# Optimization experiments

Measured on AMD Instinct MI355X. Metric: run time of the kernel, lower is better.

The kernel has to match this reference:

```python
import jax, jax.numpy as jnp
import numpy as np

B, S, E, H = 4, 2048, 1024, 16
D = E // H
LR_MULT = 100.0
EPS = 1e-5

def setup_inputs() -> dict:
    key = jax.random.key(0)
    ks = jax.random.split(key, 4)
    x = jax.random.normal(ks[0], (B, S, E), dtype=jnp.float32)
    # nn.MultiheadAttention in_proj_weight [3E,E], out_proj.weight [E,E] (bias=False)
    W_qkv = jax.random.normal(ks[1], (3 * E, E), dtype=jnp.float32) * (1.0 / np.sqrt(E))
    W_o = jax.random.normal(ks[2], (E, E), dtype=jnp.float32) * (1.0 / np.sqrt(E))
    ln_w = jnp.ones((E,), dtype=jnp.float32)
    scaler = jnp.asarray(1.0 / LR_MULT, dtype=jnp.float32)
    return {"x": x, "W_qkv": W_qkv, "W_o": W_o, "ln_w": ln_w, "scaler": scaler}

def _layernorm(x, w):
    mu = jnp.mean(x, axis=-1, keepdims=True)
    var = jnp.mean(jnp.square(x - mu), axis=-1, keepdims=True)
    return (x - mu) * jax.lax.rsqrt(var + EPS) * w

def reference(x, W_qkv, W_o, ln_w, scaler):
    resid = x
    xn = _layernorm(x, ln_w)
    qkv = jnp.einsum('bse,fe->bsf', xn, W_qkv)  # [B,S,3E]
    q, k, v = jnp.split(qkv, 3, axis=-1)
    q = q.reshape(B, S, H, D)
    k = k.reshape(B, S, H, D)
    v = v.reshape(B, S, H, D)
    scores = jnp.einsum('bihd,bjhd->bhij', q, k) / jnp.sqrt(jnp.asarray(D, x.dtype))
    # linear_encoding_base[i,j] = j - i; bias = softplus(100*scaler)*(j-i) where j<=i else -inf
    i_idx = jnp.arange(S)
    rel = (i_idx[None, :] - i_idx[:, None]).astype(x.dtype)  # j - i
    causal = i_idx[None, :] <= i_idx[:, None]                # tril: j <= i
    slope = jax.nn.softplus(LR_MULT * scaler)
    bias = jnp.where(causal, slope * rel, -jnp.inf)          # [S,S]
    att = jax.nn.softmax(scores + bias[None, None, :, :], axis=-1)
    out = jnp.einsum('bhij,bjhd->bihd', att, v).reshape(B, S, E)
    out = jnp.einsum('bse,fe->bsf', out, W_o)
    return out + resid
```

## Files before the change

kernel.cpp:

```cpp
#include <hip/hip_runtime.h>

typedef unsigned short u16;
typedef unsigned int u32;
typedef __bf16 bf16x8 __attribute__((ext_vector_type(8)));
typedef float f32x4 __attribute__((ext_vector_type(4)));

#define B_ 4
#define S_ 2048
#define E_ 1024
#define H_ 16
#define D_ 64

__device__ __forceinline__ u16 f2bf(float f) {
  u32 u = __float_as_uint(f);
  u32 r = u + 0x7fffu + ((u >> 16) & 1u);
  return (u16)(r >> 16);
}

__device__ __forceinline__ void gload16(const u16* g, u16* l) {
  __builtin_amdgcn_global_load_lds((const __attribute__((address_space(1))) void*)g,
                                   (__attribute__((address_space(3))) void*)l, 16, 0, 0);
}

__global__ __launch_bounds__(256) void ln_kernel(const float* __restrict__ x,
                                                 const float* __restrict__ w,
                                                 u16* __restrict__ xn) {
  const int lane = threadIdx.x & 63;
  const int wv = threadIdx.x >> 6;
  const int row = blockIdx.x * 4 + wv;
  const float4* xr = (const float4*)(x + (size_t)row * E_);
  float4 vv[4];
  float s = 0.f, sq = 0.f;
#pragma unroll
  for (int i = 0; i < 4; ++i) {
    vv[i] = xr[lane + i * 64];
    s += vv[i].x + vv[i].y + vv[i].z + vv[i].w;
    sq += vv[i].x * vv[i].x + vv[i].y * vv[i].y + vv[i].z * vv[i].z + vv[i].w * vv[i].w;
  }
#pragma unroll
  for (int off = 1; off < 64; off <<= 1) {
    s += __shfl_xor(s, off);
    sq += __shfl_xor(sq, off);
  }
  const float mu = s * (1.f / E_);
  const float rs = rsqrtf(sq * (1.f / E_) - mu * mu + 1e-5f);
  u16* xo = xn + (size_t)row * E_;
  const float4* wr = (const float4*)w;
#pragma unroll
  for (int i = 0; i < 4; ++i) {
    float4 w4 = wr[lane + i * 64];
    ushort4 o;
    o.x = f2bf((vv[i].x - mu) * rs * w4.x);
    o.y = f2bf((vv[i].y - mu) * rs * w4.y);
    o.z = f2bf((vv[i].z - mu) * rs * w4.z);
    o.w = f2bf((vv[i].w - mu) * rs * w4.w);
    ((ushort4*)xo)[lane + i * 64] = o;
  }
}

__global__ __launch_bounds__(256) void cvt_kernel(const float* __restrict__ src,
                                                  u16* __restrict__ dst) {
  const int i = blockIdx.x * 256 + threadIdx.x;
  float4 v = ((const float4*)src)[i];
  ushort4 o;
  o.x = f2bf(v.x);
  o.y = f2bf(v.y);
  o.z = f2bf(v.z);
  o.w = f2bf(v.w);
  ((ushort4*)dst)[i] = o;
}

__global__ __launch_bounds__(512, 2) void gemm8_qkv(const u16* __restrict__ A,
                                                    const u16* __restrict__ Bw,
                                                    u16* __restrict__ qo,
                                                    u16* __restrict__ ko,
                                                    u16* __restrict__ vo) {
  constexpr int K = 1024;
  constexpr int NT = K / 64;
  __shared__ u16 lds[2][2][256 * 64];
  const int t = threadIdx.x;
  const int lane = t & 63, wv = t >> 6;
  const int wm = wv >> 2, wn = wv & 3;
  const int d = blockIdx.y * 12 + blockIdx.x;
  const int lin = (d & 7) * 48 + (d >> 3);
  const int m0 = (lin & 31) * 256, n0 = (lin >> 5) * 256;
  const int r16 = lane & 15, g4 = lane >> 4;
  const int l3 = lane >> 3, l7 = lane & 7;
  const int colsrc = ((l7 ^ l3) * 8);

  f32x4 acc[8][4] = {};
  bf16x8 af[8][2];
  bf16x8 bfr[2][2];

  auto issue = [&](int ph, int buf, int kt) {
#pragma unroll
    for (int s = 0; s < 2; ++s) {
      const int j = wv * 2 + s;
      int c, m;
      if (ph == 0)      { m = 0; c = j + (j & 8); }
      else if (ph == 1) { m = 1; c = (j >> 2) * 8 + (j & 3); }
      else if (ph == 2) { m = 0; c = 8 + j + (j & 8); }
      else              { m = 1; c = (j >> 2) * 8 + 4 + (j & 3); }
      const u16* src = (m == 0 ? A + (size_t)(m0 + c * 8 + l3) * K
                               : Bw + (size_t)(n0 + c * 8 + l3) * K) + kt + colsrc;
      gload16(src, &lds[buf][m][c * 512]);
    }
  };

  auto loadA = [&](const u16* As, int half) {
#pragma unroll
    for (int i = 0; i < 4; ++i) {
      const int mi = half * 4 + i;
      const int r = wm * 128 + mi * 16 + r16;
      const int sw = (r & 7) << 3;
#pragma unroll
      for (int kc = 0; kc < 2; ++kc)
        af[mi][kc] = *(const bf16x8*)&As[r * 64 + ((kc * 32 + g4 * 8) ^ sw)];
    }
  };
  auto loadB = [&](const u16* Bs, int pair) {
#pragma unroll
    for (int n2 = 0; n2 < 2; ++n2) {
      const int r = wn * 64 + (pair * 2 + n2) * 16 + r16;
      const int sw = (r & 7) << 3;
#pragma unroll
      for (int kc = 0; kc < 2; ++kc)
        bfr[n2][kc] = *(const bf16x8*)&Bs[r * 64 + ((kc * 32 + g4 * 8) ^ sw)];
    }
  };
  auto mmac = [&](int mhalf, int npair) {
#pragma unroll
    for (int i = 0; i < 4; ++i)
#pragma unroll
      for (int n2 = 0; n2 < 2; ++n2)
#pragma unroll
        for (int kc = 0; kc < 2; ++kc)
          acc[mhalf * 4 + i][npair * 2 + n2] = __builtin_amdgcn_mfma_f32_16x16x32_bf16(
              af[mhalf * 4 + i][kc], bfr[n2][kc], acc[mhalf * 4 + i][npair * 2 + n2], 0, 0, 0);
  };

  issue(0, 0, 0);
  issue(1, 0, 0);
  issue(2, 0, 0);
  issue(3, 0, 0);
  asm volatile("s_waitcnt vmcnt(0)" ::: "memory");
  __builtin_amdgcn_s_barrier();

  for (int kt2 = 0; kt2 < NT - 1; ++kt2) {
    const int cur = kt2 & 1;
    const u16* As = lds[cur][0];
    const u16* Bs = lds[cur][1];
    const int ktN = (kt2 + 1) * 64;
    loadA(As, 0);
    loadB(Bs, 0);
    issue(0, cur ^ 1, ktN);
    __builtin_amdgcn_s_barrier();
    asm volatile("s_waitcnt lgkmcnt(0)" ::: "memory");
    asm volatile("s_waitcnt vmcnt(4)" ::: "memory");
    __builtin_amdgcn_sched_barrier(0);
    __builtin_amdgcn_s_setprio(1);
    mmac(0, 0);
    __builtin_amdgcn_s_setprio(0);
    __builtin_amdgcn_s_barrier();
    loadA(As, 1);
    issue(1, cur ^ 1, ktN);
    __builtin_amdgcn_s_barrier();
    asm volatile("s_waitcnt lgkmcnt(0)" ::: "memory");
    asm volatile("s_waitcnt vmcnt(4)" ::: "memory");
    __builtin_amdgcn_sched_barrier(0);
    __builtin_amdgcn_s_setprio(1);
    mmac(1, 0);
    __builtin_amdgcn_s_setprio(0);
    __builtin_amdgcn_s_barrier();
    loadB(Bs, 1);
    issue(2, cur ^ 1, ktN);
    __builtin_amdgcn_s_barrier();
    asm volatile("s_waitcnt lgkmcnt(0)" ::: "memory");
    __builtin_amdgcn_sched_barrier(0);
    __builtin_amdgcn_s_setprio(1);
    mmac(1, 1);
    __builtin_amdgcn_s_setprio(0);
    __builtin_amdgcn_s_barrier();
    issue(3, cur ^ 1, ktN);
    __builtin_amdgcn_s_barrier();
    asm volatile("s_waitcnt vmcnt(4)" ::: "memory");
    __builtin_amdgcn_sched_barrier(0);
    __builtin_amdgcn_s_setprio(1);
    mmac(0, 1);
    __builtin_amdgcn_s_setprio(0);
    __builtin_amdgcn_s_barrier();
  }
  {
    const int cur = (NT - 1) & 1;
    const u16* As = lds[cur][0];
    const u16* Bs = lds[cur][1];
    loadA(As, 0);
    loadB(Bs, 0);
    __builtin_amdgcn_s_barrier();
    asm volatile("s_waitcnt lgkmcnt(0)" ::: "memory");
    asm volatile("s_waitcnt vmcnt(2)" ::: "memory");
    __builtin_amdgcn_sched_barrier(0);
    __builtin_amdgcn_s_setprio(1);
    mmac(0, 0);
    __builtin_amdgcn_s_setprio(0);
    __builtin_amdgcn_s_barrier();
    loadA(As, 1);
    __builtin_amdgcn_s_barrier();
    asm volatile("s_waitcnt lgkmcnt(0)" ::: "memory");
    asm volatile("s_waitcnt vmcnt(0)" ::: "memory");
    __builtin_amdgcn_sched_barrier(0);
    __builtin_amdgcn_s_setprio(1);
    mmac(1, 0);
    __builtin_amdgcn_s_setprio(0);
    __builtin_amdgcn_s_barrier();
    loadB(Bs, 1);
    asm volatile("s_waitcnt lgkmcnt(0)" ::: "memory");
    __builtin_amdgcn_sched_barrier(0);
    __builtin_amdgcn_s_setprio(1);
    mmac(1, 1);
    mmac(0, 1);
    __builtin_amdgcn_s_setprio(0);
  }

  const int which = n0 >> 10;
  u16* dst = which == 0 ? qo : (which == 1 ? ko : vo);
#pragma unroll
  for (int mi = 0; mi < 8; ++mi)
#pragma unroll
    for (int e = 0; e < 4; ++e) {
      const int gr = m0 + wm * 128 + mi * 16 + g4 * 4 + e;
      const int bb = gr >> 11, ss = gr & 2047;
#pragma unroll
      for (int ni = 0; ni < 4; ++ni) {
        const int gc = n0 + wn * 64 + ni * 16 + r16;
        const int hh = (gc >> 6) & 15;
        const int dd = gc & 63;
        dst[(((size_t)bb * H_ + hh) * S_ + ss) * D_ + dd] = f2bf(acc[mi][ni][e]);
      }
    }
}

__global__ __launch_bounds__(256, 2) void gemm_bt1(const u16* __restrict__ A,
                                                   const u16* __restrict__ Bw,
                                                   const int K,
                                                   const float* __restrict__ xres,
                                                   float* __restrict__ outp) {
  __shared__ u16 lds[2][2][128 * 64];
  const int t = threadIdx.x;
  const int lane = t & 63, wv = t >> 6;
  const int wm = wv >> 1, wn = wv & 1;
  const int d = blockIdx.y * 8 + blockIdx.x;
  const int lin = (d & 7) * 64 + (d >> 3);
  const int m0 = (lin & 63) * 128, n0 = (lin >> 6) * 128;
  const int r16 = lane & 15, g4 = lane >> 4;

  const f32x4 fzero = {0.f, 0.f, 0.f, 0.f};
  f32x4 acc[4][4];
#pragma unroll
  for (int i = 0; i < 4; ++i)
#pragma unroll
    for (int j = 0; j < 4; ++j) acc[i][j] = fzero;

  const int srow8 = lane >> 3;
  const int scol = (lane & 7) * 8;

  auto stage = [&](int bu, int kt) {
#pragma unroll
    for (int i = 0; i < 4; ++i) {
      const int c = wv * 4 + i;
      const int row = c * 8 + srow8;
      gload16(A + (size_t)(m0 + row) * K + kt + scol, &lds[bu][0][c * 512]);
      gload16(Bw + (size_t)(n0 + row) * K + kt + scol, &lds[bu][1][c * 512]);
    }
  };

  auto compute = [&](int bu) {
    const u16* As = lds[bu][0];
    const u16* Bs = lds[bu][1];
    bf16x8 af[4][2], bfr[4][2];
#pragma unroll
    for (int mi = 0; mi < 4; ++mi)
#pragma unroll
      for (int kc = 0; kc < 2; ++kc)
        af[mi][kc] = *(const bf16x8*)&As[(wm * 64 + mi * 16 + r16) * 64 + kc * 32 + g4 * 8];
#pragma unroll
    for (int ni = 0; ni < 4; ++ni)
#pragma unroll
      for (int kc = 0; kc < 2; ++kc)
        bfr[ni][kc] = *(const bf16x8*)&Bs[(wn * 64 + ni * 16 + r16) * 64 + kc * 32 + g4 * 8];
#pragma unroll
    for (int mi = 0; mi < 4; ++mi)
#pragma unroll
      for (int ni = 0; ni < 4; ++ni)
#pragma unroll
        for (int kc = 0; kc < 2; ++kc)
          acc[mi][ni] = __builtin_amdgcn_mfma_f32_16x16x32_bf16(af[mi][kc], bfr[ni][kc],
                                                                acc[mi][ni], 0, 0, 0);
  };

  stage(0, 0);
  __syncthreads();
  int cur = 0;
  for (int kt = 64; kt < K; kt += 64) {
    stage(cur ^ 1, kt);
    compute(cur);
    __syncthreads();
    cur ^= 1;
  }
  compute(cur);

#pragma unroll
  for (int mi = 0; mi < 4; ++mi)
#pragma unroll
    for (int e = 0; e < 4; ++e) {
      const int gr = m0 + wm * 64 + mi * 16 + g4 * 4 + e;
#pragma unroll
      for (int ni = 0; ni < 4; ++ni) {
        const int gc = n0 + wn * 64 + ni * 16 + r16;
        const size_t idx = (size_t)gr * 1024 + gc;
        outp[idx] = acc[mi][ni][e] + xres[idx];
      }
    }
}

__global__ __launch_bounds__(256) void attn_kernel(const u16* __restrict__ q,
                                                   const u16* __restrict__ k,
                                                   const u16* __restrict__ v,
                                                   const float* __restrict__ scaler_p,
                                                   u16* __restrict__ ao) {
  __shared__ u16 Qs[64 * 72];
  __shared__ u16 Ks[64 * 72];
  __shared__ u16 Vt[64 * 72];
  __shared__ u16 Ps[4 * 16 * 72];
  const int t = threadIdx.x;
  const int lane = t & 63, wv = t >> 6;
  const int r16 = lane & 15, g4 = lane >> 4;
  const int it = blockIdx.x;
  const int bh = blockIdx.y;
  const int bb = bh >> 4, hh = bh & 15;
  const size_t base = (size_t)bh * (S_ * D_);

  const float tt = 100.f * scaler_p[0];
  const float slope = (tt > 20.f) ? tt : log1pf(expf(tt));
  const float L2E = 1.4426950408889634f;
  const float qs_l2e = 0.125f * L2E;
  const float sl_l2e = slope * L2E;
  int nb = (int)ceilf(80.f / (slope * 64.f));
  if (nb < 1) nb = 1;
  int jt0 = it - nb;
  if (jt0 < 0) jt0 = 0;

  {
    const int r = t >> 2, c = (t & 3) << 4;
    const u16* gp = q + base + (size_t)(it * 64 + r) * D_ + c;
    uint4 a0 = ((const uint4*)gp)[0];
    uint4 a1 = ((const uint4*)gp)[1];
    *(uint4*)&Qs[r * 72 + c] = a0;
    *(uint4*)&Qs[r * 72 + c + 8] = a1;
  }

  float mrun[4] = {-3e38f, -3e38f, -3e38f, -3e38f};
  float lrun[4] = {0.f, 0.f, 0.f, 0.f};
  const f32x4 fzero = {0.f, 0.f, 0.f, 0.f};
  f32x4 oacc[4];
#pragma unroll
  for (int i = 0; i < 4; ++i) oacc[i] = fzero;

  bf16x8 qa[2];
  bool qloaded = false;

  for (int jt = jt0; jt <= it; ++jt) {
    {
      const int r = t >> 2, c = (t & 3) << 4;
      const u16* kg = k + base + (size_t)(jt * 64 + r) * D_ + c;
      uint4 k0 = ((const uint4*)kg)[0];
      uint4 k1 = ((const uint4*)kg)[1];
      *(uint4*)&Ks[r * 72 + c] = k0;
      *(uint4*)&Ks[r * 72 + c + 8] = k1;
      const u16* vg = v + base + (size_t)(jt * 64 + r) * D_ + c;
      union { uint4 u; u16 s[8]; } v0, v1;
      v0.u = ((const uint4*)vg)[0];
      v1.u = ((const uint4*)vg)[1];
#pragma unroll
      for (int j = 0; j < 8; ++j) {
        Vt[(c + j) * 72 + r] = v0.s[j];
        Vt[(c + 8 + j) * 72 + r] = v1.s[j];
      }
    }
    __syncthreads();
    if (!qloaded) {
      qloaded = true;
#pragma unroll
      for (int kc = 0; kc < 2; ++kc)
        qa[kc] = *(const bf16x8*)&Qs[(wv * 16 + r16) * 72 + kc * 32 + g4 * 8];
    }
    f32x4 sfr[4];
#pragma unroll
    for (int nt = 0; nt < 4; ++nt) {
      sfr[nt] = fzero;
#pragma unroll
      for (int kc = 0; kc < 2; ++kc) {
        bf16x8 kb = *(const bf16x8*)&Ks[(nt * 16 + r16) * 72 + kc * 32 + g4 * 8];
        sfr[nt] = __builtin_amdgcn_mfma_f32_16x16x32_bf16(qa[kc], kb, sfr[nt], 0, 0, 0);
      }
    }
    const bool diag = (jt == it);
    const float jb = (float)((jt - it) * 64);
    float pm[4] = {-3e38f, -3e38f, -3e38f, -3e38f};
#pragma unroll
    for (int nt = 0; nt < 4; ++nt) {
      const int jl = nt * 16 + r16;
#pragma unroll
      for (int e = 0; e < 4; ++e) {
        const int il = wv * 16 + g4 * 4 + e;
        float sc = sfr[nt][e] * qs_l2e + sl_l2e * (jb + (float)(jl - il));
        if (diag && jl > il) sc = -3e38f;
        sfr[nt][e] = sc;
        pm[e] = fmaxf(pm[e], sc);
      }
    }
#pragma unroll
    for (int e = 0; e < 4; ++e) {
#pragma unroll
      for (int off = 1; off < 16; off <<= 1) pm[e] = fmaxf(pm[e], __shfl_xor(pm[e], off));
    }
    u16* Psw = Ps + wv * (16 * 72);
    float psum[4] = {0.f, 0.f, 0.f, 0.f};
#pragma unroll
    for (int e = 0; e < 4; ++e) {
      const float mn = fmaxf(mrun[e], pm[e]);
      const float rsc = exp2f(mrun[e] - mn);
      mrun[e] = mn;
      lrun[e] *= rsc;
#pragma unroll
      for (int nt = 0; nt < 4; ++nt) oacc[nt][e] *= rsc;
    }
#pragma unroll
    for (int nt = 0; nt < 4; ++nt)
#pragma unroll
      for (int e = 0; e < 4; ++e) {
        const float p = exp2f(sfr[nt][e] - mrun[e]);
        psum[e] += p;
        Psw[(g4 * 4 + e) * 72 + nt * 16 + r16] = f2bf(p);
      }
#pragma unroll
    for (int e = 0; e < 4; ++e) {
#pragma unroll
      for (int off = 1; off < 16; off <<= 1) psum[e] += __shfl_xor(psum[e], off);
      lrun[e] += psum[e];
    }
    bf16x8 pa[2];
#pragma unroll
    for (int jk = 0; jk < 2; ++jk)
      pa[jk] = *(const bf16x8*)&Psw[r16 * 72 + jk * 32 + g4 * 8];
#pragma unroll
    for (int nt = 0; nt < 4; ++nt)
#pragma unroll
      for (int jk = 0; jk < 2; ++jk) {
        bf16x8 vb = *(const bf16x8*)&Vt[(nt * 16 + r16) * 72 + jk * 32 + g4 * 8];
        oacc[nt] = __builtin_amdgcn_mfma_f32_16x16x32_bf16(pa[jk], vb, oacc[nt], 0, 0, 0);
      }
    __syncthreads();
  }
#pragma unroll
  for (int e = 0; e < 4; ++e) {
    const float inv = 1.f / lrun[e];
    const int row = it * 64 + wv * 16 + g4 * 4 + e;
#pragma unroll
    for (int nt = 0; nt < 4; ++nt) {
      const int col = hh * 64 + nt * 16 + r16;
      ao[((size_t)bb * S_ + row) * E_ + col] = f2bf(oacc[nt][e] * inv);
    }
  }
}

extern "C" void kernel_launch(void* const* d_in, const int* in_sizes, int n_in,
                              void* d_out, int out_size, void* d_ws, size_t ws_size,
                              hipStream_t stream) {
  const float* x = (const float*)d_in[0];
  const float* Wqkv = (const float*)d_in[1];
  const float* Wo = (const float*)d_in[2];
  const float* lnw = (const float*)d_in[3];
  const float* scaler = (const float*)d_in[4];
  float* out = (float*)d_out;
  char* ws = (char*)d_ws;

  u16* xn = (u16*)(ws + 0);
  u16* q = (u16*)(ws + 16777216);
  u16* kk = (u16*)(ws + 33554432);
  u16* vv = (u16*)(ws + 50331648);
  u16* ao = (u16*)(ws + 67108864);
  u16* wqkvb = (u16*)(ws + 83886080);
  u16* wob = (u16*)(ws + 90177536);

  ln_kernel<<<2048, 256, 0, stream>>>(x, lnw, xn);
  cvt_kernel<<<3072, 256, 0, stream>>>(Wqkv, wqkvb);
  cvt_kernel<<<1024, 256, 0, stream>>>(Wo, wob);
  gemm8_qkv<<<dim3(12, 32), 512, 0, stream>>>(xn, wqkvb, q, kk, vv);
  attn_kernel<<<dim3(32, 64), 256, 0, stream>>>(q, kk, vv, scaler, ao);
  gemm_bt1<<<dim3(8, 64), 256, 0, stream>>>(ao, wob, 1024, x, out);
}
```

Measured before the change: 137.1 us.

## Fuse prep kernels, drop tile swizzle, issue all QKV GEMM prefetches up front

Merges the layernorm and the two weight-conversion kernels into one launch, using block-index ranges to pick the job. This removes two kernel launches and their tail gaps. The QKV GEMM now issues all four next-tile global-to-LDS load phases at the start of each k-iteration, with graded vmcnt waits, instead of interleaving them between MFMA phases, and fuses the last two MFMA phases. It also replaces the XCD-aware block-index remap with a plain row/column mapping, which may hurt L2 locality across chiplets.

```diff
diff --git a/kernel.cpp b/kernel.cpp
--- a/kernel.cpp
+++ b/kernel.cpp
@@ -22,52 +22,58 @@
                                    (__attribute__((address_space(3))) void*)l, 16, 0, 0);
 }
 
-__global__ __launch_bounds__(256) void ln_kernel(const float* __restrict__ x,
-                                                 const float* __restrict__ w,
-                                                 u16* __restrict__ xn) {
-  const int lane = threadIdx.x & 63;
-  const int wv = threadIdx.x >> 6;
-  const int row = blockIdx.x * 4 + wv;
-  const float4* xr = (const float4*)(x + (size_t)row * E_);
-  float4 vv[4];
-  float s = 0.f, sq = 0.f;
-#pragma unroll
-  for (int i = 0; i < 4; ++i) {
-    vv[i] = xr[lane + i * 64];
-    s += vv[i].x + vv[i].y + vv[i].z + vv[i].w;
-    sq += vv[i].x * vv[i].x + vv[i].y * vv[i].y + vv[i].z * vv[i].z + vv[i].w * vv[i].w;
-  }
-#pragma unroll
-  for (int off = 1; off < 64; off <<= 1) {
-    s += __shfl_xor(s, off);
-    sq += __shfl_xor(sq, off);
-  }
-  const float mu = s * (1.f / E_);
-  const float rs = rsqrtf(sq * (1.f / E_) - mu * mu + 1e-5f);
-  u16* xo = xn + (size_t)row * E_;
-  const float4* wr = (const float4*)w;
-#pragma unroll
-  for (int i = 0; i < 4; ++i) {
-    float4 w4 = wr[lane + i * 64];
+__global__ __launch_bounds__(256) void prep_kernel(const float* __restrict__ x,
+                                                   const float* __restrict__ lnw,
+                                                   u16* __restrict__ xn,
+                                                   const float* __restrict__ Wqkv,
+                                                   u16* __restrict__ wqkvb,
+                                                   const float* __restrict__ Wo,
+                                                   u16* __restrict__ wob) {
+  const int b = blockIdx.x;
+  if (b < 2048) {
+    const int lane = threadIdx.x & 63;
+    const int wv = threadIdx.x >> 6;
+    const int row = b * 4 + wv;
+    const float4* xr = (const float4*)(x + (size_t)row * E_);
+    float4 vv[4];
+    float s = 0.f, sq = 0.f;
+#pragma unroll
+    for (int i = 0; i < 4; ++i) {
+      vv[i] = xr[lane + i * 64];
+      s += vv[i].x + vv[i].y + vv[i].z + vv[i].w;
+      sq += vv[i].x * vv[i].x + vv[i].y * vv[i].y + vv[i].z * vv[i].z + vv[i].w * vv[i].w;
+    }
+#pragma unroll
+    for (int off = 1; off < 64; off <<= 1) {
+      s += __shfl_xor(s, off);
+      sq += __shfl_xor(sq, off);
+    }
+    const float mu = s * (1.f / E_);
+    const float rs = rsqrtf(sq * (1.f / E_) - mu * mu + 1e-5f);
+    u16* xo = xn + (size_t)row * E_;
+    const float4* wr = (const float4*)lnw;
+#pragma unroll
+    for (int i = 0; i < 4; ++i) {
+      float4 w4 = wr[lane + i * 64];
+      ushort4 o;
+      o.x = f2bf((vv[i].x - mu) * rs * w4.x);
+      o.y = f2bf((vv[i].y - mu) * rs * w4.y);
+      o.z = f2bf((vv[i].z - mu) * rs * w4.z);
+      o.w = f2bf((vv[i].w - mu) * rs * w4.w);
+      ((ushort4*)xo)[lane + i * 64] = o;
+    }
+  } else {
+    const float* src = (b < 5120) ? Wqkv : Wo;
+    u16* dst = (b < 5120) ? wqkvb : wob;
+    const int i = (b < 5120 ? b - 2048 : b - 5120) * 256 + threadIdx.x;
+    float4 v = ((const float4*)src)[i];
     ushort4 o;
-    o.x = f2bf((vv[i].x - mu) * rs * w4.x);
-    o.y = f2bf((vv[i].y - mu) * rs * w4.y);
-    o.z = f2bf((vv[i].z - mu) * rs * w4.z);
-    o.w = f2bf((vv[i].w - mu) * rs * w4.w);
-    ((ushort4*)xo)[lane + i * 64] = o;
-  }
-}
-
-__global__ __launch_bounds__(256) void cvt_kernel(const float* __restrict__ src,
-                                                  u16* __restrict__ dst) {
-  const int i = blockIdx.x * 256 + threadIdx.x;
-  float4 v = ((const float4*)src)[i];
-  ushort4 o;
-  o.x = f2bf(v.x);
-  o.y = f2bf(v.y);
-  o.z = f2bf(v.z);
-  o.w = f2bf(v.w);
-  ((ushort4*)dst)[i] = o;
+    o.x = f2bf(v.x);
+    o.y = f2bf(v.y);
+    o.z = f2bf(v.z);
+    o.w = f2bf(v.w);
+    ((ushort4*)dst)[i] = o;
+  }
 }
 
 __global__ __launch_bounds__(512, 2) void gemm8_qkv(const u16* __restrict__ A,
@@ -81,9 +87,7 @@
   const int t = threadIdx.x;
   const int lane = t & 63, wv = t >> 6;
   const int wm = wv >> 2, wn = wv & 3;
-  const int d = blockIdx.y * 12 + blockIdx.x;
-  const int lin = (d & 7) * 48 + (d >> 3);
-  const int m0 = (lin & 31) * 256, n0 = (lin >> 5) * 256;
+  const int m0 = blockIdx.y * 256, n0 = blockIdx.x * 256;
   const int r16 = lane & 15, g4 = lane >> 4;
   const int l3 = lane >> 3, l7 = lane & 7;
   const int colsrc = ((l7 ^ l3) * 8);
@@ -154,38 +158,33 @@
     loadA(As, 0);
     loadB(Bs, 0);
     issue(0, cur ^ 1, ktN);
+    issue(1, cur ^ 1, ktN);
+    issue(2, cur ^ 1, ktN);
+    issue(3, cur ^ 1, ktN);
+    __builtin_amdgcn_s_barrier();
+    asm volatile("s_waitcnt lgkmcnt(0)" ::: "memory");
+    asm volatile("s_waitcnt vmcnt(10)" ::: "memory");
+    __builtin_amdgcn_sched_barrier(0);
+    __builtin_amdgcn_s_setprio(1);
+    mmac(0, 0);
+    __builtin_amdgcn_s_setprio(0);
+    __builtin_amdgcn_s_barrier();
+    loadA(As, 1);
+    __builtin_amdgcn_s_barrier();
+    asm volatile("s_waitcnt lgkmcnt(0)" ::: "memory");
+    asm volatile("s_waitcnt vmcnt(8)" ::: "memory");
+    __builtin_amdgcn_sched_barrier(0);
+    __builtin_amdgcn_s_setprio(1);
+    mmac(1, 0);
+    __builtin_amdgcn_s_setprio(0);
+    __builtin_amdgcn_s_barrier();
+    loadB(Bs, 1);
     __builtin_amdgcn_s_barrier();
     asm volatile("s_waitcnt lgkmcnt(0)" ::: "memory");
     asm volatile("s_waitcnt vmcnt(4)" ::: "memory");
     __builtin_amdgcn_sched_barrier(0);
     __builtin_amdgcn_s_setprio(1);
-    mmac(0, 0);
-    __builtin_amdgcn_s_setprio(0);
-    __builtin_amdgcn_s_barrier();
-    loadA(As, 1);
-    issue(1, cur ^ 1, ktN);
-    __builtin_amdgcn_s_barrier();
-    asm volatile("s_waitcnt lgkmcnt(0)" ::: "memory");
-    asm volatile("s_waitcnt vmcnt(4)" ::: "memory");
-    __builtin_amdgcn_sched_barrier(0);
-    __builtin_amdgcn_s_setprio(1);
-    mmac(1, 0);
-    __builtin_amdgcn_s_setprio(0);
-    __builtin_amdgcn_s_barrier();
-    loadB(Bs, 1);
-    issue(2, cur ^ 1, ktN);
-    __builtin_amdgcn_s_barrier();
-    asm volatile("s_waitcnt lgkmcnt(0)" ::: "memory");
-    __builtin_amdgcn_sched_barrier(0);
-    __builtin_amdgcn_s_setprio(1);
     mmac(1, 1);
-    __builtin_amdgcn_s_setprio(0);
-    __builtin_amdgcn_s_barrier();
-    issue(3, cur ^ 1, ktN);
-    __builtin_amdgcn_s_barrier();
-    asm volatile("s_waitcnt vmcnt(4)" ::: "memory");
-    __builtin_amdgcn_sched_barrier(0);
-    __builtin_amdgcn_s_setprio(1);
     mmac(0, 1);
     __builtin_amdgcn_s_setprio(0);
     __builtin_amdgcn_s_barrier();
@@ -493,9 +492,7 @@
   u16* wqkvb = (u16*)(ws + 83886080);
   u16* wob = (u16*)(ws + 90177536);
 
-  ln_kernel<<<2048, 256, 0, stream>>>(x, lnw, xn);
-  cvt_kernel<<<3072, 256, 0, stream>>>(Wqkv, wqkvb);
-  cvt_kernel<<<1024, 256, 0, stream>>>(Wo, wob);
+  prep_kernel<<<6144, 256, 0, stream>>>(x, lnw, xn, Wqkv, wqkvb, Wo, wob);
   gemm8_qkv<<<dim3(12, 32), 512, 0, stream>>>(xn, wqkvb, q, kk, vv);
   attn_kernel<<<dim3(32, 64), 256, 0, stream>>>(q, kk, vv, scaler, ao);
   gemm_bt1<<<dim3(8, 64), 256, 0, stream>>>(ao, wob, 1024, x, out);
```

Result: no change. 139.4 us (+1.7%).
